# Kernel tuning notes

Hardware: AMD Instinct MI355X
Metric: run time of the kernel (lower is better)

## Reference

```python
import jax, jax.numpy as jnp
import numpy as np

B, T, D_MODEL = 2, 2048, 2048
Q_HEADS, KV_HEADS = 16, 4
HEAD_DIM = D_MODEL // Q_HEADS  # 128
N_GROUPS = Q_HEADS // KV_HEADS  # 4
THETA = 10000.0


def setup_inputs() -> dict:
    key = jax.random.key(0)
    ks = jax.random.split(key, 5)
    s = 0.02
    return {
        "x": jax.random.normal(ks[0], (B, T, D_MODEL), dtype=jnp.float32),
        "Wq": jax.random.normal(ks[1], (Q_HEADS * HEAD_DIM, D_MODEL), dtype=jnp.float32) * s,
        "Wk": jax.random.normal(ks[2], (KV_HEADS * HEAD_DIM, D_MODEL), dtype=jnp.float32) * s,
        "Wv": jax.random.normal(ks[3], (KV_HEADS * HEAD_DIM, D_MODEL), dtype=jnp.float32) * s,
        "Wo": jax.random.normal(ks[4], (D_MODEL, D_MODEL), dtype=jnp.float32) * s,
    }


def _apply_rope(q, k, t):
    # freqs = outer(arange(t), 1/theta^(2i/d)) ; complex rotation on (even,odd) pairs
    inv_freq = 1.0 / (THETA ** (jnp.arange(0, HEAD_DIM, 2, dtype=jnp.float32) / HEAD_DIM))
    ang = jnp.arange(t, dtype=jnp.float32)[:, None] * inv_freq[None, :]  # [t, hd/2]
    cos = jnp.cos(ang)[None, :, None, :]  # [1,t,1,hd/2]
    sin = jnp.sin(ang)[None, :, None, :]

    def rot(x):
        xr = x.reshape(*x.shape[:-1], HEAD_DIM // 2, 2)
        xe, xo = xr[..., 0], xr[..., 1]
        out = jnp.stack([xe * cos - xo * sin, xe * sin + xo * cos], axis=-1)
        return out.reshape(x.shape)

    return rot(q), rot(k)


def reference(x, Wq, Wk, Wv, Wo):
    b, t, c = x.shape
    q = (x @ Wq.T).reshape(b, t, Q_HEADS, HEAD_DIM)
    k = (x @ Wk.T).reshape(b, t, KV_HEADS, HEAD_DIM)
    v = (x @ Wv.T).reshape(b, t, KV_HEADS, HEAD_DIM)
    q, k = _apply_rope(q, k, t)
    # GQA: repeat kv heads to match q heads (repeat_interleave on head dim)
    k = jnp.repeat(k, N_GROUPS, axis=2)
    v = jnp.repeat(v, N_GROUPS, axis=2)
    q = q.transpose(0, 2, 1, 3)  # [b,h,t,d]
    k = k.transpose(0, 2, 1, 3)
    v = v.transpose(0, 2, 1, 3)
    scale = HEAD_DIM ** -0.5
    attn = jnp.einsum("bhqd,bhkd->bhqk", q, k) * scale
    causal = jnp.tril(jnp.ones((t, t), dtype=bool))
    attn = jnp.where(causal[None, None], attn, -jnp.inf)
    attn = jax.nn.softmax(attn, axis=-1)
    out = jnp.einsum("bhqk,bhkd->bhqd", attn, v)
    out = out.transpose(0, 2, 1, 3).reshape(b, t, c)
    return out @ Wo.T
```

## Files before the change

kernel.cpp:

```cpp
#include <hip/hip_runtime.h>
#include <hip/hip_bf16.h>

typedef __bf16 bf16_t;
typedef __bf16 bf16x8 __attribute__((ext_vector_type(8)));
typedef __bf16 bf16x4 __attribute__((ext_vector_type(4)));
typedef float f32x4 __attribute__((ext_vector_type(4)));

#define SEQ_T 2048
#define DMODEL 2048
#define NQH 16
#define NKVH 4
#define HDIM 128

__device__ __forceinline__ f32x4 mfma16x16x32(bf16x8 a, bf16x8 b, f32x4 c) {
  return __builtin_amdgcn_mfma_f32_16x16x32_bf16(a, b, c, 0, 0, 0);
}

typedef __attribute__((address_space(3))) void lds_void_t;
typedef __attribute__((address_space(1))) const void gbl_void_t;
__device__ __forceinline__ void gload_lds16(const bf16_t* g, bf16_t* l) {
  __builtin_amdgcn_global_load_lds((gbl_void_t*)g, (lds_void_t*)l, 16, 0, 0);
}
__device__ __forceinline__ void BAR() {
  asm volatile("" ::: "memory");
  __builtin_amdgcn_s_barrier();
  asm volatile("" ::: "memory");
}

__global__ __launch_bounds__(256) void cast_all(const float* __restrict__ x,
                                                const float* __restrict__ Wq,
                                                const float* __restrict__ Wk,
                                                const float* __restrict__ Wv,
                                                const float* __restrict__ Wo,
                                                bf16_t* __restrict__ xb,
                                                bf16_t* __restrict__ Wqkvb,
                                                bf16_t* __restrict__ Wob) {
  const int idx = blockIdx.x * 256 + threadIdx.x;
  const float* src;
  bf16_t* dst;
  if (idx < 1048576) {
    src = x + (size_t)idx * 8;
    dst = xb + (size_t)idx * 8;
  } else if (idx < 1572864) {
    const int r = idx - 1048576;
    src = Wq + (size_t)r * 8;
    dst = Wqkvb + (size_t)r * 8;
  } else if (idx < 1703936) {
    const int r = idx - 1572864;
    src = Wk + (size_t)r * 8;
    dst = Wqkvb + 4194304 + (size_t)r * 8;
  } else if (idx < 1835008) {
    const int r = idx - 1703936;
    src = Wv + (size_t)r * 8;
    dst = Wqkvb + 5242880 + (size_t)r * 8;
  } else {
    const int r = idx - 1835008;
    src = Wo + (size_t)r * 8;
    dst = Wob + (size_t)r * 8;
  }
  const float4* s4 = reinterpret_cast<const float4*>(src);
  float4 a = s4[0], b = s4[1];
  bf16x8 r8 = {(bf16_t)a.x, (bf16_t)a.y, (bf16_t)a.z, (bf16_t)a.w,
               (bf16_t)b.x, (bf16_t)b.y, (bf16_t)b.z, (bf16_t)b.w};
  *reinterpret_cast<bf16x8*>(dst) = r8;
}

__global__ __launch_bounds__(256) void sincos_kernel(float2* __restrict__ tab) {
  int idx = blockIdx.x * 256 + threadIdx.x;
  int t = idx >> 6, i = idx & 63;
  float inv = exp2f((float)i * (-13.287712379549449f / 64.0f));
  float ang = (float)t * inv;
  float s, c;
  sincosf(ang, &s, &c);
  tab[idx] = make_float2(c, s);
}

__global__ __launch_bounds__(512, 2) void gemm_qkv(const bf16_t* __restrict__ A,
                                                   const bf16_t* __restrict__ W,
                                                   bf16_t* __restrict__ q_out,
                                                   bf16_t* __restrict__ k_out,
                                                   bf16_t* __restrict__ v_out,
                                                   const float2* __restrict__ tab) {
  constexpr int K = 2048;
  constexpr int NT = 32;
  const int id = ((int)blockIdx.x & 7) * 32 + ((int)blockIdx.x >> 3);
  const int m0 = (id >> 4) * 256, n0 = (id & 15) * 192;
  const int tid = threadIdx.x;
  const int lane = tid & 63, w = tid >> 6;
  const int wr = w >> 2, wc = w & 3;
  const int l15 = lane & 15, g = lane >> 4;
  __shared__ bf16_t smem[2][(256 + 192) * 64];
  f32x4 acc[8][3] = {};
  bf16x8 af[4][2], bfr[3][2];

  auto ISSUE_A = [&](int tt, int h) {
    bf16_t* base = &smem[tt & 1][0] + h * (128 * 64);
    const bf16_t* src = A + (size_t)(m0 + h * 128) * K + tt * 64;
#pragma unroll
    for (int i = 0; i < 2; i++) {
      const int rl = i * 64 + (tid >> 3);
      gload_lds16(src + (size_t)rl * K + (((tid & 7) ^ (rl & 7)) << 3),
                  base + (i * 64 + w * 8) * 64);
    }
  };
  auto ISSUE_B = [&](int tt, int c) {
    bf16_t* base = &smem[tt & 1][0] + (256 + c * 64) * 64;
    const int rl = tid >> 3;
    const bf16_t* src = W + (size_t)(n0 + c * 64 + rl) * K + tt * 64;
    gload_lds16(src + (((tid & 7) ^ (rl & 7)) << 3), base + (w * 8) * 64);
  };
  auto RDA = [&](const bf16_t* Ab, int qm) {
#pragma unroll
    for (int fi = 0; fi < 4; fi++) {
      const int row = wr * 128 + qm * 64 + fi * 16 + l15;
#pragma unroll
      for (int ksl = 0; ksl < 2; ksl++)
        af[fi][ksl] = *reinterpret_cast<const bf16x8*>(
            Ab + row * 64 + ((((ksl << 2) + g) ^ (row & 7)) << 3));
    }
  };
  auto RDB1 = [&](const bf16_t* Bb, int fj) {
    const int row = wc * 48 + fj * 16 + l15;
#pragma unroll
    for (int ksl = 0; ksl < 2; ksl++)
      bfr[fj][ksl] = *reinterpret_cast<const bf16x8*>(
          Bb + row * 64 + ((((ksl << 2) + g) ^ (row & 7)) << 3));
  };

#define MMX(QM, FJLO, FJHI)                                                   \
  do {                                                                        \
    __builtin_amdgcn_s_setprio(1);                                            \
    _Pragma("unroll") for (int fi = 0; fi < 4; fi++)                          \
        _Pragma("unroll") for (int fj = (FJLO); fj <= (FJHI); fj++)           \
            _Pragma("unroll") for (int ksl = 0; ksl < 2; ksl++)               \
                acc[(QM)*4 + fi][fj] =                                        \
                    mfma16x16x32(af[fi][ksl], bfr[fj][ksl], acc[(QM)*4 + fi][fj]); \
    __builtin_amdgcn_s_setprio(0);                                            \
  } while (0)

  ISSUE_A(0, 0);
  ISSUE_A(0, 1);
  ISSUE_B(0, 0);
  ISSUE_B(0, 1);
  ISSUE_B(0, 2);

  for (int t = 0; t < NT; t++) {
    const bf16_t* Ab = &smem[t & 1][0];
    const bf16_t* Bb = Ab + 256 * 64;
    if (t + 1 < NT) {
      ISSUE_A(t + 1, 0);
      ISSUE_A(t + 1, 1);
      asm volatile("s_waitcnt vmcnt(4)" ::: "memory");
    } else {
      asm volatile("s_waitcnt vmcnt(0)" ::: "memory");
    }
    BAR();
    RDA(Ab, 0);
    RDB1(Bb, 0);
    RDB1(Bb, 1);
    MMX(0, 0, 1);
    BAR();
    RDB1(Bb, 2);
    if (t + 1 < NT) {
      ISSUE_B(t + 1, 0);
      ISSUE_B(t + 1, 1);
      ISSUE_B(t + 1, 2);
    }
    BAR();
    MMX(0, 2, 2);
    BAR();
    RDA(Ab, 1);
    BAR();
    MMX(1, 0, 1);
    MMX(1, 2, 2);
    BAR();
  }
#undef MMX

#pragma unroll
  for (int fm = 0; fm < 8; fm++) {
    const int r0 = m0 + wr * 128 + fm * 16 + (g << 2);
    const int bb = r0 >> 11;
    const int tt = r0 & 2047;
#pragma unroll
    for (int fn = 0; fn < 3; fn++) {
      const int col = n0 + wc * 48 + fn * 16 + l15;
      const f32x4 v = acc[fm][fn];
      if (col < 2048) {
        const int dd = col & 127;
        const float2* tp = tab + (size_t)tt * 64 + (dd >> 1);
        bf16_t* dst = q_out + (((size_t)(bb * NQH + (col >> 7)) * SEQ_T + tt) * HDIM + dd);
#pragma unroll
        for (int i = 0; i < 4; i++) {
          float me = v[i];
          float ot = __shfl_xor(me, 1);
          float2 cs = tp[(size_t)i * 64];
          float r = (dd & 1) ? (me * cs.x + ot * cs.y) : (me * cs.x - ot * cs.y);
          dst[(size_t)i * HDIM] = (bf16_t)r;
        }
      } else if (col < 2560) {
        const int dd = col & 127;
        const float2* tp = tab + (size_t)tt * 64 + (dd >> 1);
        bf16_t* dst = k_out + (((size_t)(bb * NKVH + ((col - 2048) >> 7)) * SEQ_T + tt) * HDIM + dd);
#pragma unroll
        for (int i = 0; i < 4; i++) {
          float me = v[i];
          float ot = __shfl_xor(me, 1);
          float2 cs = tp[(size_t)i * 64];
          float r = (dd & 1) ? (me * cs.x + ot * cs.y) : (me * cs.x - ot * cs.y);
          dst[(size_t)i * HDIM] = (bf16_t)r;
        }
      } else {
        const int vc = col - 2560;
        const int hh = vc >> 7, dd = vc & 127;
        const int tp64 = (tt & ~63) | (((tt >> 2) & 3) << 4) | (((tt >> 4) & 3) << 2);
        bf16x4 pk = {(bf16_t)v[0], (bf16_t)v[1], (bf16_t)v[2], (bf16_t)v[3]};
        *reinterpret_cast<bf16x4*>(v_out + (((size_t)(bb * NKVH + hh) * HDIM + dd) * SEQ_T + tp64)) = pk;
      }
    }
  }
}

__global__ __launch_bounds__(512, 2) void gemm_out(const bf16_t* __restrict__ A,
                                                   const bf16_t* __restrict__ W,
                                                   float* __restrict__ c_out) {
  constexpr int K = 2048;
  constexpr int NT = 32;
  const int id = ((int)blockIdx.x & 7) * 32 + ((int)blockIdx.x >> 3);
  const int m0 = (id >> 4) * 256, n0 = (id & 15) * 128;
  const int tid = threadIdx.x;
  const int lane = tid & 63, w = tid >> 6;
  const int wr = w >> 2, wc = w & 3;
  const int l15 = lane & 15, g = lane >> 4;
  __shared__ bf16_t smem[2][(256 + 128) * 64];
  f32x4 acc[8][2] = {};
  bf16x8 af[4][2], bfr[1][2];

  auto ISSUE_HALF = [&](int tt, int h) {
    const int k0 = tt * 64;
    bf16_t* base = &smem[tt & 1][0] + ((h < 2) ? h * (128 * 64) : 256 * 64);
    const bf16_t* src = (h < 2) ? (A + (size_t)(m0 + h * 128) * K)
                                : (W + (size_t)n0 * K);
#pragma unroll
    for (int i = 0; i < 2; i++) {
      const int rl = i * 64 + (tid >> 3);
      gload_lds16(src + (size_t)rl * K + k0 + (((tid & 7) ^ (rl & 7)) << 3),
                  base + (i * 64 + w * 8) * 64);
    }
  };
  auto RDA = [&](const bf16_t* Ab, int qm) {
#pragma unroll
    for (int fi = 0; fi < 4; fi++) {
      const int row = wr * 128 + qm * 64 + fi * 16 + l15;
#pragma unroll
      for (int ksl = 0; ksl < 2; ksl++)
        af[fi][ksl] = *reinterpret_cast<const bf16x8*>(
            Ab + row * 64 + ((((ksl << 2) + g) ^ (row & 7)) << 3));
    }
  };
  auto RDB = [&](const bf16_t* Bb, int qn) {
    const int row = wc * 32 + qn * 16 + l15;
#pragma unroll
    for (int ksl = 0; ksl < 2; ksl++)
      bfr[0][ksl] = *reinterpret_cast<const bf16x8*>(
          Bb + row * 64 + ((((ksl << 2) + g) ^ (row & 7)) << 3));
  };

#define MMPH(QM, QN)                                                          \
  do {                                                                        \
    __builtin_amdgcn_s_setprio(1);                                            \
    _Pragma("unroll") for (int fi = 0; fi < 4; fi++)                          \
        _Pragma("unroll") for (int ksl = 0; ksl < 2; ksl++)                   \
            acc[(QM)*4 + fi][(QN)] =                                          \
                mfma16x16x32(af[fi][ksl], bfr[0][ksl], acc[(QM)*4 + fi][(QN)]); \
    __builtin_amdgcn_s_setprio(0);                                            \
  } while (0)

#pragma unroll
  for (int h = 0; h < 3; h++) ISSUE_HALF(0, h);

  for (int t = 0; t < NT; t++) {
    const bf16_t* Ab = &smem[t & 1][0];
    const bf16_t* Bb = Ab + 256 * 64;
    if (t + 1 < NT) {
      ISSUE_HALF(t + 1, 0);
      ISSUE_HALF(t + 1, 1);
      asm volatile("s_waitcnt vmcnt(4)" ::: "memory");
    } else {
      asm volatile("s_waitcnt vmcnt(0)" ::: "memory");
    }
    BAR();
    RDA(Ab, 0);
    RDB(Bb, 0);
    MMPH(0, 0);
    BAR();
    RDB(Bb, 1);
    if (t + 1 < NT) ISSUE_HALF(t + 1, 2);
    BAR();
    MMPH(0, 1);
    BAR();
    RDA(Ab, 1);
    BAR();
    MMPH(1, 1);
    BAR();
    RDB(Bb, 0);
    BAR();
    MMPH(1, 0);
    BAR();
  }
#undef MMPH

#pragma unroll
  for (int fm = 0; fm < 8; fm++) {
    const int r0 = m0 + wr * 128 + fm * 16 + (g << 2);
#pragma unroll
    for (int fn = 0; fn < 2; fn++) {
      const int col = n0 + wc * 32 + fn * 16 + l15;
#pragma unroll
      for (int i = 0; i < 4; i++) c_out[(size_t)(r0 + i) * 2048 + col] = acc[fm][fn][i];
    }
  }
}

__global__ __launch_bounds__(256, 2) void attn_kernel(const bf16_t* __restrict__ Qb,
                                                      const bf16_t* __restrict__ Kb,
                                                      const bf16_t* __restrict__ Vt,
                                                      bf16_t* __restrict__ AO) {
  const int bx = blockIdx.x;
  const int b = bx >> 3, hp = bx & 7;
  const int h0 = hp << 1;
  const int kvh = h0 >> 2;
  const int by = blockIdx.y;
  const int j = (by < 16) ? (31 - by) : (by - 16);
  const int q0 = j * 64;
  const int tid = threadIdx.x;
  const int lane = tid & 63, w = tid >> 6;
  const int l15 = lane & 15, g = lane >> 4;
  const bf16_t* Qp0 = Qb + (size_t)(b * NQH + h0) * SEQ_T * HDIM;
  const bf16_t* Qp1 = Qp0 + (size_t)SEQ_T * HDIM;
  const bf16_t* Kp = Kb + (size_t)(b * NKVH + kvh) * SEQ_T * HDIM;
  const bf16_t* Vp = Vt + (size_t)(b * NKVH + kvh) * HDIM * SEQ_T;
  __shared__ bf16_t smem[2][16384];
  const int qr = q0 + w * 16 + l15;
  bf16x8 qfA[4], qfB[4];
#pragma unroll
  for (int c = 0; c < 4; c++) {
    qfA[c] = *reinterpret_cast<const bf16x8*>(Qp0 + (size_t)qr * HDIM + c * 32 + (g << 3));
    qfB[c] = *reinterpret_cast<const bf16x8*>(Qp1 + (size_t)qr * HDIM + c * 32 + (g << 3));
  }
  f32x4 oA[8] = {}, oB[8] = {};
  float mA = -1e30f, lA = 0.0f, mB = -1e30f, lB = 0.0f;
  const float kscale = 0.08838834764831845f * 1.4426950408889634f;
  const int ntiles = j + 1;

  auto STAGE = [&](int it, int buf) {
    const int kv0s = it * 64;
    bf16_t* Ks = smem[buf];
    bf16_t* Vs = smem[buf] + 8192;
#pragma unroll
    for (int cc = 0; cc < 4; cc++) {
      const int ck = cc * 256 + tid;
      const int krow = ck >> 4, kg = ck & 15;
      gload_lds16(Kp + (size_t)(kv0s + krow) * HDIM + ((kg ^ (krow & 7)) << 3),
                  Ks + (cc * 256 + w * 64) * 8);
      const int vrow = ck >> 3, vg = ck & 7;
      gload_lds16(Vp + (size_t)vrow * SEQ_T + kv0s + ((vg ^ (vrow & 7)) << 3),
                  Vs + (cc * 256 + w * 64) * 8);
    }
  };

  auto SOFTMAX = [&](float* sv, float& m, float& l, f32x4* o, bf16x8* pc) {
    float a0 = fmaxf(fmaxf(sv[0], sv[1]), fmaxf(sv[2], sv[3]));
    float a1 = fmaxf(fmaxf(sv[4], sv[5]), fmaxf(sv[6], sv[7]));
    float a2 = fmaxf(fmaxf(sv[8], sv[9]), fmaxf(sv[10], sv[11]));
    float a3 = fmaxf(fmaxf(sv[12], sv[13]), fmaxf(sv[14], sv[15]));
    float tm = fmaxf(fmaxf(a0, a1), fmaxf(a2, a3));
    tm = fmaxf(tm, __shfl_xor(tm, 16, 64));
    tm = fmaxf(tm, __shfl_xor(tm, 32, 64));
    tm *= kscale;
    if (!__all(tm <= m + 8.0f)) {
      const float mnew = fmaxf(m, tm);
      const float alpha = exp2f(m - mnew);
      m = mnew;
      l *= alpha;
#pragma unroll
      for (int dt = 0; dt < 8; dt++) o[dt] *= alpha;
    }
#pragma unroll
    for (int jj = 0; jj < 16; jj++) sv[jj] = exp2f(__builtin_fmaf(sv[jj], kscale, -m));
    float r0 = (sv[0] + sv[1]) + (sv[2] + sv[3]);
    float r1 = (sv[4] + sv[5]) + (sv[6] + sv[7]);
    float r2 = (sv[8] + sv[9]) + (sv[10] + sv[11]);
    float r3 = (sv[12] + sv[13]) + (sv[14] + sv[15]);
    float rs = (r0 + r1) + (r2 + r3);
    rs += __shfl_xor(rs, 16, 64);
    rs += __shfl_xor(rs, 32, 64);
    l += rs;
#pragma unroll
    for (int s = 0; s < 2; s++) {
      bf16x8 t = {(bf16_t)sv[8 * s],     (bf16_t)sv[8 * s + 1], (bf16_t)sv[8 * s + 2],
                  (bf16_t)sv[8 * s + 3], (bf16_t)sv[8 * s + 4], (bf16_t)sv[8 * s + 5],
                  (bf16_t)sv[8 * s + 6], (bf16_t)sv[8 * s + 7]};
      pc[s] = t;
    }
  };

  auto COMPUTE = [&](const bf16_t* Ks, const bf16_t* Vs, int kv0) {
    float svA[16], svB[16];
    const bool noMask = (kv0 != q0);
    __builtin_amdgcn_s_setprio(1);
#pragma unroll
    for (int ksub = 0; ksub < 4; ksub++) {
      f32x4 sa = {}, sb = {};
      const int krow = ksub * 16 + l15;
#pragma unroll
      for (int ch = 0; ch < 4; ch++) {
        bf16x8 kf = *reinterpret_cast<const bf16x8*>(
            Ks + krow * 128 + ((((ch << 2) + g) ^ (krow & 7)) << 3));
        sa = mfma16x16x32(kf, qfA[ch], sa);
        sb = mfma16x16x32(kf, qfB[ch], sb);
      }
      if (noMask) {
#pragma unroll
        for (int i = 0; i < 4; i++) { svA[ksub * 4 + i] = sa[i]; svB[ksub * 4 + i] = sb[i]; }
      } else {
        const int dlt = qr - kv0 - ksub * 16 - (g << 2);
#pragma unroll
        for (int i = 0; i < 4; i++) {
          svA[ksub * 4 + i] = (i <= dlt) ? sa[i] : -3e38f;
          svB[ksub * 4 + i] = (i <= dlt) ? sb[i] : -3e38f;
        }
      }
    }
    __builtin_amdgcn_s_setprio(0);
    bf16x8 pcA[2], pcB[2];
    SOFTMAX(svA, mA, lA, oA, pcA);
    SOFTMAX(svB, mB, lB, oB, pcB);
    __builtin_amdgcn_s_setprio(1);
#pragma unroll
    for (int dt = 0; dt < 8; dt++) {
      const int vrow = dt * 16 + l15;
#pragma unroll
      for (int s = 0; s < 2; s++) {
        bf16x8 vv = *reinterpret_cast<const bf16x8*>(
            Vs + vrow * 64 + (((2 * g + s) ^ (vrow & 7)) << 3));
        oA[dt] = mfma16x16x32(vv, pcA[s], oA[dt]);
        oB[dt] = mfma16x16x32(vv, pcB[s], oB[dt]);
      }
    }
    __builtin_amdgcn_s_setprio(0);
  };

  STAGE(0, 0);
  for (int it = 0; it < ntiles; it++) {
    const int buf = it & 1;
    if (it + 1 < ntiles) {
      STAGE(it + 1, buf ^ 1);
      asm volatile("s_waitcnt vmcnt(8)" ::: "memory");
    } else {
      asm volatile("s_waitcnt vmcnt(0)" ::: "memory");
    }
    BAR();
    COMPUTE(smem[buf], smem[buf] + 8192, it * 64);
    BAR();
  }
  bf16_t* os = &smem[0][0] + w * 2048;
  auto EPI = [&](f32x4* o, float lsum, int h) {
    const float linv = 1.0f / lsum;
#pragma unroll
    for (int dt = 0; dt < 8; dt++) {
      bf16x4 pk = {(bf16_t)(o[dt][0] * linv), (bf16_t)(o[dt][1] * linv),
                   (bf16_t)(o[dt][2] * linv), (bf16_t)(o[dt][3] * linv)};
      *reinterpret_cast<bf16x4*>(os + l15 * 128 + dt * 16 + (g << 2)) = pk;
    }
    const size_t rowb = (size_t)b * SEQ_T + q0 + w * 16;
#pragma unroll
    for (int kk = 0; kk < 4; kk++) {
      const int c = lane + kk * 64;
      const int q = c >> 4, gc = c & 15;
      *reinterpret_cast<bf16x8*>(AO + (rowb + q) * DMODEL + h * HDIM + gc * 8) =
          *reinterpret_cast<const bf16x8*>(os + q * 128 + gc * 8);
    }
  };
  EPI(oA, lA, h0);
  EPI(oB, lB, h0 + 1);
}

extern "C" void kernel_launch(void* const* d_in, const int* in_sizes, int n_in,
                              void* d_out, int out_size, void* d_ws, size_t ws_size,
                              hipStream_t stream) {
  const float* x = (const float*)d_in[0];
  const float* Wq = (const float*)d_in[1];
  const float* Wk = (const float*)d_in[2];
  const float* Wv = (const float*)d_in[3];
  const float* Wo = (const float*)d_in[4];
  float* out = (float*)d_out;
  char* ws = (char*)d_ws;
  bf16_t* xb = (bf16_t*)(ws);
  bf16_t* Wqkvb = (bf16_t*)(ws + 16777216);
  bf16_t* Wob = (bf16_t*)(ws + 29360128);
  bf16_t* Qb = (bf16_t*)(ws + 37748736);
  bf16_t* Kb = (bf16_t*)(ws + 54525952);
  bf16_t* Vt = (bf16_t*)(ws + 58720256);
  bf16_t* AO = (bf16_t*)(ws + 62914560);
  float2* tab = (float2*)(ws + 79691776);

  cast_all<<<9216, 256, 0, stream>>>(x, Wq, Wk, Wv, Wo, xb, Wqkvb, Wob);
  sincos_kernel<<<512, 256, 0, stream>>>(tab);
  gemm_qkv<<<256, 512, 0, stream>>>(xb, Wqkvb, Qb, Kb, Vt, tab);
  attn_kernel<<<dim3(16, 32), 256, 0, stream>>>(Qb, Kb, Vt, AO);
  gemm_out<<<256, 512, 0, stream>>>(AO, Wob, out);
}
```

Baseline: 186.1 us.

## Attention: one head per block, 32-wide KV tiles, per-wave causal skip

Restructures the attention kernel so each block handles one query head instead of two, with KV tiles shrunk from 64 to 32 keys and LDS halved. The V transpose permutation in the QKV GEMM epilogue is changed to match the 32-key tile layout. Waves skip tiles entirely past their causal limit, and the grid doubles with higher occupancy (4 blocks/CU) and a new q-block ordering for load balance. This gives up the K/V sharing between two heads in exchange for more parallelism and less wasted masked work, at the cost of more K/V global traffic and more barriers per key.

```diff
diff --git a/kernel.cpp b/kernel.cpp
--- a/kernel.cpp
+++ b/kernel.cpp
@@ -213,9 +213,9 @@
       } else {
         const int vc = col - 2560;
         const int hh = vc >> 7, dd = vc & 127;
-        const int tp64 = (tt & ~63) | (((tt >> 2) & 3) << 4) | (((tt >> 4) & 3) << 2);
+        const int tp32 = (tt & ~31) | (((tt >> 2) & 3) << 3) | (((tt >> 4) & 1) << 2);
         bf16x4 pk = {(bf16_t)v[0], (bf16_t)v[1], (bf16_t)v[2], (bf16_t)v[3]};
-        *reinterpret_cast<bf16x4*>(v_out + (((size_t)(bb * NKVH + hh) * HDIM + dd) * SEQ_T + tp64)) = pk;
+        *reinterpret_cast<bf16x4*>(v_out + (((size_t)(bb * NKVH + hh) * HDIM + dd) * SEQ_T + tp32)) = pk;
       }
     }
   }
@@ -322,131 +322,100 @@
   }
 }
 
-__global__ __launch_bounds__(256, 2) void attn_kernel(const bf16_t* __restrict__ Qb,
+__global__ __launch_bounds__(256, 4) void attn_kernel(const bf16_t* __restrict__ Qb,
                                                       const bf16_t* __restrict__ Kb,
                                                       const bf16_t* __restrict__ Vt,
                                                       bf16_t* __restrict__ AO) {
-  const int bx = blockIdx.x;
-  const int b = bx >> 3, hp = bx & 7;
-  const int h0 = hp << 1;
-  const int kvh = h0 >> 2;
+  const int bh = blockIdx.x;
+  const int b = bh >> 4, h = bh & 15, kvh = h >> 2;
   const int by = blockIdx.y;
-  const int j = (by < 16) ? (31 - by) : (by - 16);
+  const int r = by & 7, qd = by >> 3;
+  const int j = (qd == 0) ? (31 - r) : (qd == 1) ? r : (qd == 2) ? (16 + r) : (15 - r);
   const int q0 = j * 64;
   const int tid = threadIdx.x;
   const int lane = tid & 63, w = tid >> 6;
   const int l15 = lane & 15, g = lane >> 4;
-  const bf16_t* Qp0 = Qb + (size_t)(b * NQH + h0) * SEQ_T * HDIM;
-  const bf16_t* Qp1 = Qp0 + (size_t)SEQ_T * HDIM;
+  const bf16_t* Qp = Qb + (size_t)(b * NQH + h) * SEQ_T * HDIM;
   const bf16_t* Kp = Kb + (size_t)(b * NKVH + kvh) * SEQ_T * HDIM;
   const bf16_t* Vp = Vt + (size_t)(b * NKVH + kvh) * HDIM * SEQ_T;
-  __shared__ bf16_t smem[2][16384];
+  __shared__ bf16_t smem[2][8192];
   const int qr = q0 + w * 16 + l15;
-  bf16x8 qfA[4], qfB[4];
-#pragma unroll
-  for (int c = 0; c < 4; c++) {
-    qfA[c] = *reinterpret_cast<const bf16x8*>(Qp0 + (size_t)qr * HDIM + c * 32 + (g << 3));
-    qfB[c] = *reinterpret_cast<const bf16x8*>(Qp1 + (size_t)qr * HDIM + c * 32 + (g << 3));
-  }
-  f32x4 oA[8] = {}, oB[8] = {};
-  float mA = -1e30f, lA = 0.0f, mB = -1e30f, lB = 0.0f;
+  bf16x8 qf[4];
+#pragma unroll
+  for (int c = 0; c < 4; c++)
+    qf[c] = *reinterpret_cast<const bf16x8*>(Qp + (size_t)qr * HDIM + c * 32 + (g << 3));
+  f32x4 o[8] = {};
+  float mrun = -1e30f, lsum = 0.0f;
   const float kscale = 0.08838834764831845f * 1.4426950408889634f;
-  const int ntiles = j + 1;
+  const int ntiles = 2 * j + 2;
+  const int wlim = q0 + w * 16 + 15;
 
   auto STAGE = [&](int it, int buf) {
-    const int kv0s = it * 64;
+    const int kv0s = it * 32;
     bf16_t* Ks = smem[buf];
-    bf16_t* Vs = smem[buf] + 8192;
-#pragma unroll
-    for (int cc = 0; cc < 4; cc++) {
+    bf16_t* Vs = smem[buf] + 4096;
+#pragma unroll
+    for (int cc = 0; cc < 2; cc++) {
       const int ck = cc * 256 + tid;
       const int krow = ck >> 4, kg = ck & 15;
       gload_lds16(Kp + (size_t)(kv0s + krow) * HDIM + ((kg ^ (krow & 7)) << 3),
                   Ks + (cc * 256 + w * 64) * 8);
-      const int vrow = ck >> 3, vg = ck & 7;
-      gload_lds16(Vp + (size_t)vrow * SEQ_T + kv0s + ((vg ^ (vrow & 7)) << 3),
+      const int vrow = ck >> 2, vg = ck & 3;
+      gload_lds16(Vp + (size_t)vrow * SEQ_T + kv0s + ((vg ^ (vrow & 3)) << 3),
                   Vs + (cc * 256 + w * 64) * 8);
     }
   };
 
-  auto SOFTMAX = [&](float* sv, float& m, float& l, f32x4* o, bf16x8* pc) {
-    float a0 = fmaxf(fmaxf(sv[0], sv[1]), fmaxf(sv[2], sv[3]));
-    float a1 = fmaxf(fmaxf(sv[4], sv[5]), fmaxf(sv[6], sv[7]));
-    float a2 = fmaxf(fmaxf(sv[8], sv[9]), fmaxf(sv[10], sv[11]));
-    float a3 = fmaxf(fmaxf(sv[12], sv[13]), fmaxf(sv[14], sv[15]));
-    float tm = fmaxf(fmaxf(a0, a1), fmaxf(a2, a3));
+  auto COMPUTE = [&](const bf16_t* Ks, const bf16_t* Vs, int kv0) {
+    float sv[8];
+    const bool noMask = (kv0 + 31 <= q0 + w * 16);
+    __builtin_amdgcn_s_setprio(1);
+#pragma unroll
+    for (int ksub = 0; ksub < 2; ksub++) {
+      f32x4 sa = {};
+      const int krow = ksub * 16 + l15;
+#pragma unroll
+      for (int ch = 0; ch < 4; ch++) {
+        bf16x8 kf = *reinterpret_cast<const bf16x8*>(
+            Ks + krow * 128 + ((((ch << 2) + g) ^ (krow & 7)) << 3));
+        sa = mfma16x16x32(kf, qf[ch], sa);
+      }
+      if (noMask) {
+#pragma unroll
+        for (int i = 0; i < 4; i++) sv[ksub * 4 + i] = sa[i];
+      } else {
+        const int dlt = qr - kv0 - ksub * 16 - (g << 2);
+#pragma unroll
+        for (int i = 0; i < 4; i++) sv[ksub * 4 + i] = (i <= dlt) ? sa[i] : -3e38f;
+      }
+    }
+    __builtin_amdgcn_s_setprio(0);
+    float t0 = fmaxf(fmaxf(sv[0], sv[1]), fmaxf(sv[2], sv[3]));
+    float t1 = fmaxf(fmaxf(sv[4], sv[5]), fmaxf(sv[6], sv[7]));
+    float tm = fmaxf(t0, t1);
     tm = fmaxf(tm, __shfl_xor(tm, 16, 64));
     tm = fmaxf(tm, __shfl_xor(tm, 32, 64));
     tm *= kscale;
-    if (!__all(tm <= m + 8.0f)) {
-      const float mnew = fmaxf(m, tm);
-      const float alpha = exp2f(m - mnew);
-      m = mnew;
-      l *= alpha;
+    if (!__all(tm <= mrun + 8.0f)) {
+      const float mnew = fmaxf(mrun, tm);
+      const float alpha = exp2f(mrun - mnew);
+      mrun = mnew;
+      lsum *= alpha;
 #pragma unroll
       for (int dt = 0; dt < 8; dt++) o[dt] *= alpha;
     }
 #pragma unroll
-    for (int jj = 0; jj < 16; jj++) sv[jj] = exp2f(__builtin_fmaf(sv[jj], kscale, -m));
-    float r0 = (sv[0] + sv[1]) + (sv[2] + sv[3]);
-    float r1 = (sv[4] + sv[5]) + (sv[6] + sv[7]);
-    float r2 = (sv[8] + sv[9]) + (sv[10] + sv[11]);
-    float r3 = (sv[12] + sv[13]) + (sv[14] + sv[15]);
-    float rs = (r0 + r1) + (r2 + r3);
-    rs += __shfl_xor(rs, 16, 64);
-    rs += __shfl_xor(rs, 32, 64);
-    l += rs;
-#pragma unroll
-    for (int s = 0; s < 2; s++) {
-      bf16x8 t = {(bf16_t)sv[8 * s],     (bf16_t)sv[8 * s + 1], (bf16_t)sv[8 * s + 2],
-                  (bf16_t)sv[8 * s + 3], (bf16_t)sv[8 * s + 4], (bf16_t)sv[8 * s + 5],
-                  (bf16_t)sv[8 * s + 6], (bf16_t)sv[8 * s + 7]};
-      pc[s] = t;
-    }
-  };
-
-  auto COMPUTE = [&](const bf16_t* Ks, const bf16_t* Vs, int kv0) {
-    float svA[16], svB[16];
-    const bool noMask = (kv0 != q0);
-    __builtin_amdgcn_s_setprio(1);
-#pragma unroll
-    for (int ksub = 0; ksub < 4; ksub++) {
-      f32x4 sa = {}, sb = {};
-      const int krow = ksub * 16 + l15;
-#pragma unroll
-      for (int ch = 0; ch < 4; ch++) {
-        bf16x8 kf = *reinterpret_cast<const bf16x8*>(
-            Ks + krow * 128 + ((((ch << 2) + g) ^ (krow & 7)) << 3));
-        sa = mfma16x16x32(kf, qfA[ch], sa);
-        sb = mfma16x16x32(kf, qfB[ch], sb);
-      }
-      if (noMask) {
-#pragma unroll
-        for (int i = 0; i < 4; i++) { svA[ksub * 4 + i] = sa[i]; svB[ksub * 4 + i] = sb[i]; }
-      } else {
-        const int dlt = qr - kv0 - ksub * 16 - (g << 2);
-#pragma unroll
-        for (int i = 0; i < 4; i++) {
-          svA[ksub * 4 + i] = (i <= dlt) ? sa[i] : -3e38f;
-          svB[ksub * 4 + i] = (i <= dlt) ? sb[i] : -3e38f;
-        }
-      }
-    }
-    __builtin_amdgcn_s_setprio(0);
-    bf16x8 pcA[2], pcB[2];
-    SOFTMAX(svA, mA, lA, oA, pcA);
-    SOFTMAX(svB, mB, lB, oB, pcB);
+    for (int jj = 0; jj < 8; jj++) sv[jj] = exp2f(__builtin_fmaf(sv[jj], kscale, -mrun));
+    lsum += ((sv[0] + sv[1]) + (sv[2] + sv[3])) + ((sv[4] + sv[5]) + (sv[6] + sv[7]));
+    bf16x8 pc = {(bf16_t)sv[0], (bf16_t)sv[1], (bf16_t)sv[2], (bf16_t)sv[3],
+                 (bf16_t)sv[4], (bf16_t)sv[5], (bf16_t)sv[6], (bf16_t)sv[7]};
     __builtin_amdgcn_s_setprio(1);
 #pragma unroll
     for (int dt = 0; dt < 8; dt++) {
       const int vrow = dt * 16 + l15;
-#pragma unroll
-      for (int s = 0; s < 2; s++) {
-        bf16x8 vv = *reinterpret_cast<const bf16x8*>(
-            Vs + vrow * 64 + (((2 * g + s) ^ (vrow & 7)) << 3));
-        oA[dt] = mfma16x16x32(vv, pcA[s], oA[dt]);
-        oB[dt] = mfma16x16x32(vv, pcB[s], oB[dt]);
-      }
+      bf16x8 vv = *reinterpret_cast<const bf16x8*>(
+          Vs + vrow * 32 + ((g ^ (vrow & 3)) << 3));
+      o[dt] = mfma16x16x32(vv, pc, o[dt]);
     }
     __builtin_amdgcn_s_setprio(0);
   };
@@ -456,34 +425,33 @@
     const int buf = it & 1;
     if (it + 1 < ntiles) {
       STAGE(it + 1, buf ^ 1);
-      asm volatile("s_waitcnt vmcnt(8)" ::: "memory");
+      asm volatile("s_waitcnt vmcnt(4)" ::: "memory");
     } else {
       asm volatile("s_waitcnt vmcnt(0)" ::: "memory");
     }
     BAR();
-    COMPUTE(smem[buf], smem[buf] + 8192, it * 64);
-    BAR();
-  }
+    const int kv0 = it * 32;
+    if (kv0 <= wlim) COMPUTE(smem[buf], smem[buf] + 4096, kv0);
+    BAR();
+  }
+  lsum += __shfl_xor(lsum, 16, 64);
+  lsum += __shfl_xor(lsum, 32, 64);
+  const float linv = 1.0f / lsum;
   bf16_t* os = &smem[0][0] + w * 2048;
-  auto EPI = [&](f32x4* o, float lsum, int h) {
-    const float linv = 1.0f / lsum;
-#pragma unroll
-    for (int dt = 0; dt < 8; dt++) {
-      bf16x4 pk = {(bf16_t)(o[dt][0] * linv), (bf16_t)(o[dt][1] * linv),
-                   (bf16_t)(o[dt][2] * linv), (bf16_t)(o[dt][3] * linv)};
-      *reinterpret_cast<bf16x4*>(os + l15 * 128 + dt * 16 + (g << 2)) = pk;
-    }
-    const size_t rowb = (size_t)b * SEQ_T + q0 + w * 16;
-#pragma unroll
-    for (int kk = 0; kk < 4; kk++) {
-      const int c = lane + kk * 64;
-      const int q = c >> 4, gc = c & 15;
-      *reinterpret_cast<bf16x8*>(AO + (rowb + q) * DMODEL + h * HDIM + gc * 8) =
-          *reinterpret_cast<const bf16x8*>(os + q * 128 + gc * 8);
-    }
-  };
-  EPI(oA, lA, h0);
-  EPI(oB, lB, h0 + 1);
+#pragma unroll
+  for (int dt = 0; dt < 8; dt++) {
+    bf16x4 pk = {(bf16_t)(o[dt][0] * linv), (bf16_t)(o[dt][1] * linv),
+                 (bf16_t)(o[dt][2] * linv), (bf16_t)(o[dt][3] * linv)};
+    *reinterpret_cast<bf16x4*>(os + l15 * 128 + dt * 16 + (g << 2)) = pk;
+  }
+  const size_t rowb = (size_t)b * SEQ_T + q0 + w * 16;
+#pragma unroll
+  for (int kk = 0; kk < 4; kk++) {
+    const int c = lane + kk * 64;
+    const int q = c >> 4, gc = c & 15;
+    *reinterpret_cast<bf16x8*>(AO + (rowb + q) * DMODEL + h * HDIM + gc * 8) =
+        *reinterpret_cast<const bf16x8*>(os + q * 128 + gc * 8);
+  }
 }
 
 extern "C" void kernel_launch(void* const* d_in, const int* in_sizes, int n_in,
@@ -508,6 +476,6 @@
   cast_all<<<9216, 256, 0, stream>>>(x, Wq, Wk, Wv, Wo, xb, Wqkvb, Wob);
   sincos_kernel<<<512, 256, 0, stream>>>(tab);
   gemm_qkv<<<256, 512, 0, stream>>>(xb, Wqkvb, Qb, Kb, Vt, tab);
-  attn_kernel<<<dim3(16, 32), 256, 0, stream>>>(Qb, Kb, Vt, AO);
+  attn_kernel<<<dim3(32, 32), 256, 0, stream>>>(Qb, Kb, Vt, AO);
   gemm_out<<<256, 512, 0, stream>>>(AO, Wob, out);
 }
```

Result: slower. 193.7 us (+4.1%).
